# Optimization experiments

Hardware: AMD Instinct MI355X
Metric: run time of the kernel (lower is better)

## Reference

```python
import jax, jax.numpy as jnp
import numpy as np

N_E, N_IN = 1024, 64
HIDDEN, OUT = 128, 64


def setup_inputs() -> dict:
    key = jax.random.key(0)
    kx, k1, k2 = jax.random.split(key, 3)
    x = jax.random.normal(kx, (N_E, N_IN), dtype=jnp.float32)
    # edge-MLP params: Dense(2*n_in -> HIDDEN) + tanh + Dense(HIDDEN -> OUT)
    W1 = jax.random.normal(k1, (2 * N_IN, HIDDEN), dtype=jnp.float32) / np.sqrt(2 * N_IN)
    b1 = jnp.zeros((HIDDEN,), dtype=jnp.float32)
    W2 = jax.random.normal(k2, (HIDDEN, OUT), dtype=jnp.float32) / np.sqrt(HIDDEN)
    b2 = jnp.zeros((OUT,), dtype=jnp.float32)
    return {"x": x, "W1": W1, "b1": b1, "W2": W2, "b2": b2}


def reference(x, W1, b1, W2, b2):
    n_e, n_in = x.shape
    # modular all-pairs index: partner of i is (i + j) % n_e for j in 1..n_e-1
    pair_idx = (jnp.arange(n_e)[:, None] + jnp.arange(1, n_e)[None, :]) % n_e  # [n_e, n_e-1]
    # pairs[i, j] = concat(x[i], x[pair_idx[i, j]])  -> [n_e, n_e-1, 2*n_in]
    self_feat = jnp.broadcast_to(x[:, None, :], (n_e, n_e - 1, n_in))
    pairs = jnp.concatenate([self_feat, x[pair_idx]], axis=-1)
    # edge MLP: Dense + tanh + Dense
    h = jnp.tanh(jnp.einsum("epf,fh->eph", pairs, W1) + b1)
    upd = jnp.einsum("eph,ho->epo", h, W2) + b2
    # mean over partners
    return jnp.mean(upd, axis=1)  # [n_e, OUT]
```

## Files before the change

kernel.cpp:

```cpp
#include <hip/hip_runtime.h>


#define N_E  1024
#define NIN  64
#define HID  128
#define OUTD 64
#define PCH  30
#define NQ   32
#define S_CH 5.5f

static constexpr float INV_S     = 1.0f / 5.5f;
static constexpr float TWO_LOG2E = 2.8853900817779268f;
static constexpr float PI_F      = 3.14159265358979323846f;

__device__ __forceinline__ float tanh_fast(float u) {
  return 1.0f - 2.0f * __builtin_amdgcn_rcpf(
      1.0f + __builtin_amdgcn_exp2f(u * TWO_LOG2E));
}

__global__ __launch_bounds__(256) void prep_coeff_kernel(
    const float* __restrict__ x, const float* __restrict__ W1,
    const float* __restrict__ b1,
    float* __restrict__ A, float* __restrict__ B,
    float* __restrict__ C, float* __restrict__ M) {
  const int t = threadIdx.x;
  if (blockIdx.x < N_E / 2) {
    __shared__ float xs[2][NIN];
    const int sub = t >> 7, h = t & (HID - 1);
    const int i = blockIdx.x * 2 + sub;
    if (t < 2 * NIN) xs[t >> 6][t & 63] = x[(blockIdx.x * 2 + (t >> 6)) * NIN + (t & 63)];
    __syncthreads();
    float accA = 0.f, accB = 0.f;
    #pragma unroll 8
    for (int f = 0; f < NIN; ++f) {
      const float xv = xs[sub][f];
      accA += xv * W1[f * HID + h];
      accB += xv * W1[(NIN + f) * HID + h];
    }
    A[i * HID + h] = accA;
    B[i * HID + h] = accB + b1[h];
  } else {
    __shared__ float ctab[NQ + 1];
    __shared__ float fg[(NQ + 1) * (NQ + 2)];
    __shared__ float G[PCH * (NQ + 2)];
    if (t <= NQ) ctab[t] = cosf((float)t * (PI_F / (float)NQ));
    for (int idx = t; idx < PCH * HID; idx += 256) M[idx] = 0.f;
    __syncthreads();
    for (int idx = t; idx < (NQ + 1) * (NQ + 1); idx += 256) {
      const int j = idx / (NQ + 1), l = idx % (NQ + 1);
      fg[j * (NQ + 2) + l] = tanh_fast(S_CH * (ctab[j] + ctab[l]));
    }
    __syncthreads();
    for (int idx = t; idx < PCH * (NQ + 1); idx += 256) {
      const int q = idx / (NQ + 1), j = idx % (NQ + 1);
      const float cphi = ctab[q];
      float c0 = 1.f, c1 = cphi;
      float s = 0.5f * fg[j * (NQ + 2) + 0];
      for (int l = 1; l <= NQ; ++l) {
        const float w = (l == NQ) ? 0.5f : 1.0f;
        s += w * fg[j * (NQ + 2) + l] * c1;
        const float c2 = 2.f * cphi * c1 - c0; c0 = c1; c1 = c2;
      }
      G[q * (NQ + 2) + j] = s;
    }
    __syncthreads();
    for (int idx = t; idx < PCH * PCH; idx += 256) {
      const int p = idx / PCH, q = idx % PCH;
      const float cphi = ctab[p];
      float c0 = 1.f, c1 = cphi;
      float s = 0.5f * G[q * (NQ + 2) + 0];
      for (int j = 1; j <= NQ; ++j) {
        const float w = (j == NQ) ? 0.5f : 1.0f;
        s += w * G[q * (NQ + 2) + j] * c1;
        const float c2 = 2.f * cphi * c1 - c0; c0 = c1; c1 = c2;
      }
      const float cp = (p == 0 ? 1.f : 2.f) / (float)NQ;
      const float cq = (q == 0 ? 1.f : 2.f) / (float)NQ;
      C[p * PCH + q] = s * cp * cq;
    }
  }
}

__global__ __launch_bounds__(256) void moments_kernel(
    const float* __restrict__ B, float* __restrict__ M) {
  __shared__ float Msub[PCH][256];
  const int t = threadIdx.x;
  const int h = t & (HID - 1), sub = t >> 7;
  float acc[PCH];
  #pragma unroll
  for (int q = 0; q < PCH; ++q) acc[q] = 0.f;
  const int k0 = blockIdx.x * 16 + sub * 8;
  for (int j = 0; j < 8; ++j) {
    float b = B[(k0 + j) * HID + h];
    b = fminf(fmaxf(b, -S_CH), S_CH) * INV_S;
    float t0 = 1.f, t1 = b;
    const float b2x = b + b;
    acc[0] += 1.f;
    acc[1] += b;
    #pragma unroll
    for (int q = 2; q < PCH; ++q) {
      const float t2 = b2x * t1 - t0;
      acc[q] += t2;
      t0 = t1; t1 = t2;
    }
  }
  #pragma unroll
  for (int q = 0; q < PCH; ++q) Msub[q][t] = acc[q];
  __syncthreads();
  for (int idx = t; idx < PCH * HID; idx += 256) {
    const int q = idx / HID, hh = idx % HID;
    atomicAdd(&M[q * HID + hh], Msub[q][hh] + Msub[q][hh + HID]);
  }
}

__global__ __launch_bounds__(HID) void v_kernel(
    const float* __restrict__ C, const float* __restrict__ M,
    float* __restrict__ V) {
  const int p = blockIdx.x, h = threadIdx.x;
  float acc = 0.f;
  #pragma unroll
  for (int q = 0; q < PCH; ++q) acc += C[p * PCH + q] * M[q * HID + h];
  V[p * HID + h] = acc;
}

__global__ __launch_bounds__(HID) void combine_out_kernel(
    const float* __restrict__ A, const float* __restrict__ B,
    const float* __restrict__ V, const float* __restrict__ W2,
    const float* __restrict__ b2, float* __restrict__ out) {
  __shared__ float Sl[HID];
  __shared__ float red[2][OUTD];
  const int i = blockIdx.x, h = threadIdx.x;
  const float ar = A[i * HID + h], br = B[i * HID + h];
  const float a = fminf(fmaxf(ar, -S_CH), S_CH) * INV_S;
  float t0 = 1.f, t1 = a;
  const float a2x = a + a;
  float acc = V[h] + a * V[HID + h];
  #pragma unroll
  for (int p = 2; p < PCH; ++p) {
    const float t2 = a2x * t1 - t0;
    acc += t2 * V[p * HID + h];
    t0 = t1; t1 = t2;
  }
  const float ts = tanh_fast(ar + br);
  Sl[h] = (acc - ts) * (1.f / (float)(N_E - 1));
  __syncthreads();
  const int o = h & (OUTD - 1), half = h >> 6;
  const int h0 = half * 64;
  float po = 0.f;
  #pragma unroll 16
  for (int hh = 0; hh < 64; ++hh)
    po += Sl[h0 + hh] * W2[(h0 + hh) * OUTD + o];
  red[half][o] = po;
  __syncthreads();
  if (h < OUTD) out[i * OUTD + h] = red[0][h] + red[1][h] + b2[h];
}

extern "C" void kernel_launch(void* const* d_in, const int* in_sizes, int n_in,
                              void* d_out, int out_size, void* d_ws, size_t ws_size,
                              hipStream_t stream) {
  const float* x  = (const float*)d_in[0];
  const float* W1 = (const float*)d_in[1];
  const float* b1 = (const float*)d_in[2];
  const float* W2 = (const float*)d_in[3];
  const float* b2 = (const float*)d_in[4];
  float* out = (float*)d_out;

  float* A = (float*)d_ws;
  float* B = A + N_E * HID;
  float* M = B + N_E * HID;
  float* V = M + PCH * HID;
  float* C = V + PCH * HID;

  prep_coeff_kernel<<<N_E / 2 + 1, 256, 0, stream>>>(x, W1, b1, A, B, C, M);
  moments_kernel<<<N_E / 16, 256, 0, stream>>>(B, M);
  v_kernel<<<PCH, HID, 0, stream>>>(C, M, V);
  combine_out_kernel<<<N_E, HID, 0, stream>>>(A, B, V, W2, b2, out);
}
```

Measured before the change: 76.43 us.

## Fuse moment accumulation into prep and V matmul into combine kernel

Folds the Chebyshev moment accumulation into the projection kernel, which now handles four rows per block. Atomics are spread over four replicated accumulators to cut contention. The V = C·M product moves into the final combine kernel, where each block recomputes V in shared memory and then processes four rows. Four launches become a memset plus two kernels, at the cost of every combine block redundantly recomputing the 30x128 V matrix.

```diff
diff --git a/kernel.cpp b/kernel.cpp
--- a/kernel.cpp
+++ b/kernel.cpp
@@ -8,6 +8,7 @@
 #define PCH  30
 #define NQ   32
 #define S_CH 5.5f
+#define NCOPY 4
 
 static constexpr float INV_S     = 1.0f / 5.5f;
 static constexpr float TWO_LOG2E = 2.8853900817779268f;
@@ -18,33 +19,57 @@
       1.0f + __builtin_amdgcn_exp2f(u * TWO_LOG2E));
 }
 
-__global__ __launch_bounds__(256) void prep_coeff_kernel(
+__global__ __launch_bounds__(256) void prep_kernel(
     const float* __restrict__ x, const float* __restrict__ W1,
     const float* __restrict__ b1,
     float* __restrict__ A, float* __restrict__ B,
-    float* __restrict__ C, float* __restrict__ M) {
+    float* __restrict__ C, float* __restrict__ M4) {
   const int t = threadIdx.x;
-  if (blockIdx.x < N_E / 2) {
-    __shared__ float xs[2][NIN];
-    const int sub = t >> 7, h = t & (HID - 1);
-    const int i = blockIdx.x * 2 + sub;
-    if (t < 2 * NIN) xs[t >> 6][t & 63] = x[(blockIdx.x * 2 + (t >> 6)) * NIN + (t & 63)];
+  if (blockIdx.x < N_E / 4) {
+    __shared__ float xs[4][NIN];
+    __shared__ float Msub[PCH][256];
+    const int h = t & (HID - 1), sub = t >> 7;
+    const int r0 = blockIdx.x * 4 + sub * 2;
+    xs[t >> 6][t & 63] = x[(blockIdx.x * 4 + (t >> 6)) * NIN + (t & 63)];
     __syncthreads();
-    float accA = 0.f, accB = 0.f;
+    float aA0 = 0.f, aA1 = 0.f, aB0 = 0.f, aB1 = 0.f;
     #pragma unroll 8
     for (int f = 0; f < NIN; ++f) {
-      const float xv = xs[sub][f];
-      accA += xv * W1[f * HID + h];
-      accB += xv * W1[(NIN + f) * HID + h];
+      const float wa = W1[f * HID + h];
+      const float wb = W1[(NIN + f) * HID + h];
+      const float x0 = xs[sub * 2][f], x1 = xs[sub * 2 + 1][f];
+      aA0 += x0 * wa; aA1 += x1 * wa;
+      aB0 += x0 * wb; aB1 += x1 * wb;
     }
-    A[i * HID + h] = accA;
-    B[i * HID + h] = accB + b1[h];
+    const float bb = b1[h];
+    const float B0 = aB0 + bb, B1 = aB1 + bb;
+    A[r0 * HID + h] = aA0; A[(r0 + 1) * HID + h] = aA1;
+    B[r0 * HID + h] = B0;  B[(r0 + 1) * HID + h] = B1;
+    const float c0v = fminf(fmaxf(B0, -S_CH), S_CH) * INV_S;
+    const float c1v = fminf(fmaxf(B1, -S_CH), S_CH) * INV_S;
+    float m[PCH];
+    m[0] = 2.f; m[1] = c0v + c1v;
+    float u0 = 1.f, u1 = c0v, v0 = 1.f, v1 = c1v;
+    const float u2x = c0v + c0v, v2x = c1v + c1v;
+    #pragma unroll
+    for (int q = 2; q < PCH; ++q) {
+      const float u2 = u2x * u1 - u0, v2 = v2x * v1 - v0;
+      m[q] = u2 + v2;
+      u0 = u1; u1 = u2; v0 = v1; v1 = v2;
+    }
+    #pragma unroll
+    for (int q = 0; q < PCH; ++q) Msub[q][t] = m[q];
+    __syncthreads();
+    const int cpy = (blockIdx.x & (NCOPY - 1)) * (PCH * HID);
+    for (int idx = t; idx < PCH * HID; idx += 256) {
+      const int q = idx >> 7, hh = idx & (HID - 1);
+      atomicAdd(&M4[cpy + idx], Msub[q][hh] + Msub[q][hh + HID]);
+    }
   } else {
     __shared__ float ctab[NQ + 1];
     __shared__ float fg[(NQ + 1) * (NQ + 2)];
     __shared__ float G[PCH * (NQ + 2)];
     if (t <= NQ) ctab[t] = cosf((float)t * (PI_F / (float)NQ));
-    for (int idx = t; idx < PCH * HID; idx += 256) M[idx] = 0.f;
     __syncthreads();
     for (int idx = t; idx < (NQ + 1) * (NQ + 1); idx += 256) {
       const int j = idx / (NQ + 1), l = idx % (NQ + 1);
@@ -81,78 +106,58 @@
   }
 }
 
-__global__ __launch_bounds__(256) void moments_kernel(
-    const float* __restrict__ B, float* __restrict__ M) {
-  __shared__ float Msub[PCH][256];
+__global__ __launch_bounds__(512) void combine_kernel(
+    const float* __restrict__ A, const float* __restrict__ B,
+    const float* __restrict__ M4, const float* __restrict__ C,
+    const float* __restrict__ W2, const float* __restrict__ b2,
+    float* __restrict__ out) {
+  __shared__ float Cs[PCH * PCH];
+  __shared__ float Ms[PCH * HID];
+  __shared__ float Vl[PCH * HID];
+  __shared__ float Sl[4][HID];
+  __shared__ float red[4][2][OUTD];
   const int t = threadIdx.x;
-  const int h = t & (HID - 1), sub = t >> 7;
-  float acc[PCH];
-  #pragma unroll
-  for (int q = 0; q < PCH; ++q) acc[q] = 0.f;
-  const int k0 = blockIdx.x * 16 + sub * 8;
-  for (int j = 0; j < 8; ++j) {
-    float b = B[(k0 + j) * HID + h];
-    b = fminf(fmaxf(b, -S_CH), S_CH) * INV_S;
-    float t0 = 1.f, t1 = b;
-    const float b2x = b + b;
-    acc[0] += 1.f;
-    acc[1] += b;
+  for (int idx = t; idx < PCH * PCH; idx += 512) Cs[idx] = C[idx];
+  for (int idx = t; idx < PCH * HID; idx += 512)
+    Ms[idx] = M4[idx] + M4[PCH * HID + idx] +
+              M4[2 * PCH * HID + idx] + M4[3 * PCH * HID + idx];
+  __syncthreads();
+  for (int idx = t; idx < PCH * HID; idx += 512) {
+    const int p = idx >> 7, hh = idx & (HID - 1);
+    float acc = 0.f;
     #pragma unroll
-    for (int q = 2; q < PCH; ++q) {
-      const float t2 = b2x * t1 - t0;
-      acc[q] += t2;
-      t0 = t1; t1 = t2;
-    }
+    for (int q = 0; q < PCH; ++q) acc += Cs[p * PCH + q] * Ms[q * HID + hh];
+    Vl[idx] = acc;
   }
-  #pragma unroll
-  for (int q = 0; q < PCH; ++q) Msub[q][t] = acc[q];
   __syncthreads();
-  for (int idx = t; idx < PCH * HID; idx += 256) {
-    const int q = idx / HID, hh = idx % HID;
-    atomicAdd(&M[q * HID + hh], Msub[q][hh] + Msub[q][hh + HID]);
-  }
-}
-
-__global__ __launch_bounds__(HID) void v_kernel(
-    const float* __restrict__ C, const float* __restrict__ M,
-    float* __restrict__ V) {
-  const int p = blockIdx.x, h = threadIdx.x;
-  float acc = 0.f;
-  #pragma unroll
-  for (int q = 0; q < PCH; ++q) acc += C[p * PCH + q] * M[q * HID + h];
-  V[p * HID + h] = acc;
-}
-
-__global__ __launch_bounds__(HID) void combine_out_kernel(
-    const float* __restrict__ A, const float* __restrict__ B,
-    const float* __restrict__ V, const float* __restrict__ W2,
-    const float* __restrict__ b2, float* __restrict__ out) {
-  __shared__ float Sl[HID];
-  __shared__ float red[2][OUTD];
-  const int i = blockIdx.x, h = threadIdx.x;
+  const int h = t & (HID - 1), row = t >> 7;
+  const int i = blockIdx.x * 4 + row;
   const float ar = A[i * HID + h], br = B[i * HID + h];
   const float a = fminf(fmaxf(ar, -S_CH), S_CH) * INV_S;
   float t0 = 1.f, t1 = a;
   const float a2x = a + a;
-  float acc = V[h] + a * V[HID + h];
+  float acc = Vl[h] + a * Vl[HID + h];
   #pragma unroll
   for (int p = 2; p < PCH; ++p) {
     const float t2 = a2x * t1 - t0;
-    acc += t2 * V[p * HID + h];
+    acc += t2 * Vl[p * HID + h];
     t0 = t1; t1 = t2;
   }
   const float ts = tanh_fast(ar + br);
-  Sl[h] = (acc - ts) * (1.f / (float)(N_E - 1));
+  Sl[row][h] = (acc - ts) * (1.f / (float)(N_E - 1));
   __syncthreads();
-  const int o = h & (OUTD - 1), half = h >> 6;
+  const int o = t & (OUTD - 1), half = (t >> 6) & 1, r2 = t >> 7;
   const int h0 = half * 64;
   float po = 0.f;
   #pragma unroll 16
   for (int hh = 0; hh < 64; ++hh)
-    po += Sl[h0 + hh] * W2[(h0 + hh) * OUTD + o];
-  red[half][o] = po;
+    po += Sl[r2][h0 + hh] * W2[(h0 + hh) * OUTD + o];
+  red[r2][half][o] = po;
   __syncthreads();
-  if (h < OUTD) out[i * OUTD + h] = red[0][h] + red[1][h] + b2[h];
+  if (t < 4 * OUTD) {
+    const int rr = t >> 6, oo = t & (OUTD - 1);
+    out[(blockIdx.x * 4 + rr) * OUTD + oo] = red[rr][0][oo] + red[rr][1][oo] + b2[oo];
+  }
 }
 
 extern "C" void kernel_launch(void* const* d_in, const int* in_sizes, int n_in,
@@ -165,14 +170,12 @@
   const float* b2 = (const float*)d_in[4];
   float* out = (float*)d_out;
 
-  float* A = (float*)d_ws;
-  float* B = A + N_E * HID;
-  float* M = B + N_E * HID;
-  float* V = M + PCH * HID;
-  float* C = V + PCH * HID;
+  float* A  = (float*)d_ws;
+  float* B  = A + N_E * HID;
+  float* M4 = B + N_E * HID;
+  float* C  = M4 + NCOPY * PCH * HID;
 
-  prep_coeff_kernel<<<N_E / 2 + 1, 256, 0, stream>>>(x, W1, b1, A, B, C, M);
-  moments_kernel<<<N_E / 16, 256, 0, stream>>>(B, M);
-  v_kernel<<<PCH, HID, 0, stream>>>(C, M, V);
-  combine_out_kernel<<<N_E, HID, 0, stream>>>(A, B, V, W2, b2, out);
+  hipMemsetAsync((void*)M4, 0, NCOPY * PCH * HID * sizeof(float), stream);
+  prep_kernel<<<N_E / 4 + 1, 256, 0, stream>>>(x, W1, b1, A, B, C, M4);
+  combine_kernel<<<N_E / 4, 512, 0, stream>>>(A, B, M4, C, W2, b2, out);
 }
```

New measurement: 77.75 us. About the same (+1.7%).
